# Kernel optimization log

Measured on AMD Instinct MI355X. Metric: run time of the kernel, lower is better.

Reference implementation:

```python
import jax, jax.numpy as jnp
import numpy as np

NEG_CLAMP = -100.0  # torch F.binary_cross_entropy clamps log terms at -100


def _ccl_labels(fg):
    """4-connectivity connected-component labeling of a [H,W] bool mask.
    Labels are assigned in raster-scan first-encounter order, matching
    scipy.ndimage.label with the default structure. Background = 0.
    Implemented as min-index label propagation to a fixed point: each
    component ends up tagged with the min flat index of its pixels (its
    first raster-scan pixel), then roots are ranked by cumsum to get 1..num.
    """
    H, W = fg.shape
    INF = H * W  # sentinel larger than any flat index
    idx = jnp.arange(INF, dtype=jnp.int32).reshape(H, W)
    init = jnp.where(fg, idx, INF)

    def step(x):
        up = jnp.concatenate([x[1:], jnp.full((1, W), INF, x.dtype)], axis=0)
        down = jnp.concatenate([jnp.full((1, W), INF, x.dtype), x[:-1]], axis=0)
        left = jnp.concatenate([x[:, 1:], jnp.full((H, 1), INF, x.dtype)], axis=1)
        right = jnp.concatenate([jnp.full((H, 1), INF, x.dtype), x[:, :-1]], axis=1)
        m = jnp.minimum(jnp.minimum(up, down), jnp.minimum(left, right))
        return jnp.where(fg, jnp.minimum(x, m), INF)

    def cond(carry):
        return carry[1]

    def body(carry):
        x, _ = carry
        nx = step(x)
        return nx, jnp.any(nx != x)

    x, _ = jax.lax.while_loop(cond, body, (init, jnp.array(True)))

    flat = x.reshape(-1)
    fgf = fg.reshape(-1)
    # a pixel is the root of its component iff its propagated tag == its own index
    is_root = fgf & (flat == jnp.arange(INF, dtype=jnp.int32))
    rank = jnp.cumsum(is_root.astype(jnp.int32))  # rank[r] = scipy label of root r
    labels = jnp.where(fgf, rank[jnp.clip(flat, 0, INF - 1)], 0)
    return labels.reshape(H, W)


def _target_map(fg):
    """Replicates: labels == labels.flatten()[1:].argmax() + 1 (faithful to source,
    including its quirky use of argmax position as the selected label value)."""
    labels = _ccl_labels(fg)
    lf = labels.reshape(-1)
    v = jnp.argmax(lf[1:]) + 1  # first occurrence of max, like numpy argmax
    return (labels == v).astype(jnp.float32)


def setup_inputs() -> dict:
    key = jax.random.key(0)
    pred = jax.random.uniform(key, (32, 1, 512, 512), dtype=jnp.float32)
    return {"pred": pred}


def reference(pred):
    fg = pred[:, 0] >= 0.5  # [N,H,W] bool
    target = jax.vmap(_target_map)(fg)[:, None]  # [N,1,H,W] float
    logp = jnp.maximum(jnp.log(pred), NEG_CLAMP)
    log1mp = jnp.maximum(jnp.log1p(-pred), NEG_CLAMP)
    return -jnp.mean(target * logp + (1.0 - target) * log1mp)
```

## Files before the change

kernel.cpp:

```cpp
#include <hip/hip_runtime.h>
#include <math.h>

#define IMG_W 512
#define IMG_H 512
#define HW (IMG_W * IMG_H)
#define LOGHW 18
#define NIMG 32
#define NTOT (NIMG * HW)
#define TILE 64
#define TPI 64
#define NTILE (NIMG * TPI)
#define EDGE_N (NTILE * 64)
#define NPAIR (NIMG * 112)
#define RTSTRIDE 2048

__device__ __forceinline__ void uf_unite(int* L, int a, int b) {
    while (true) {
        int p = ((volatile int*)L)[a];
        while (p != a) { a = p; p = ((volatile int*)L)[a]; }
        p = ((volatile int*)L)[b];
        while (p != b) { b = p; p = ((volatile int*)L)[b]; }
        if (a == b) return;
        if (a < b) { int t = a; a = b; b = t; }
        int old = atomicMin(&L[a], b);
        if (old == a) return;
        a = old;
    }
}

__global__ __launch_bounds__(512) void k_local(const float* __restrict__ pred,
                                               int* __restrict__ L,
                                               float* __restrict__ partials,
                                               int* __restrict__ edges,
                                               int* __restrict__ rootCnt,
                                               int* __restrict__ rootList,
                                               unsigned int* __restrict__ counter) {
    __shared__ int lab[TILE * TILE];
    __shared__ float swf[8];
    __shared__ int rootc;
    int tile = blockIdx.x;
    int img = tile >> 6;
    int t = tile & (TPI - 1);
    int ty = t >> 3, tx = t & 7;
    int baseLocal = (ty * TILE) * IMG_W + tx * TILE;
    const float* pi = pred + ((size_t)img << LOGHW);
    int* Li = L + ((size_t)img << LOGHW);
    int tid = threadIdx.x;
    int lane = tid & 63, wave = tid >> 6;
    if (tid == 0) rootc = 0;

    float acc = 0.0f;
#pragma unroll
    for (int j = 0; j < 8; j++) {
        int row = wave + j * 8;
        float p = pi[baseLocal + row * IMG_W + lane];
        acc += fmaxf(__logf(1.0f - p), -100.0f);
        bool fg = (p >= 0.5f);
        unsigned long long bal = __ballot(fg);
        unsigned long long starts = bal & ~(bal << 1);
        unsigned long long maskle =
            (lane == 63) ? ~0ULL : ((1ULL << (lane + 1)) - 1ULL);
        int lb = -1;
        if (fg) {
            unsigned long long pre = starts & maskle;
            lb = row * TILE + (63 - __builtin_clzll(pre));
        }
        lab[row * TILE + lane] = lb;
    }
    __syncthreads();
#pragma unroll
    for (int j = 0; j < 8; j++) {
        int row = wave + j * 8;
        if (row == 0) continue;
        int i = row * TILE + lane;
        bool c = (lab[i] >= 0) && (lab[i - TILE] >= 0);
        unsigned long long cb = __ballot(c);
        unsigned long long cs = cb & ~(cb << 1);
        if ((cs >> lane) & 1ULL) uf_unite(lab, i, i - TILE);
    }
    __syncthreads();
    int* rl = rootList + (size_t)tile * RTSTRIDE;
#pragma unroll
    for (int j = 0; j < 8; j++) {
        int row = wave + j * 8;
        int i = row * TILE + lane;
        bool fg = (lab[i] >= 0);
        unsigned long long bal = __ballot(fg);
        unsigned long long st = bal & ~(bal << 1);
        if ((st >> lane) & 1ULL) {
            int x = i, p = lab[x];
            while (p != x) {
                int g = lab[p];
                lab[x] = g;
                x = g;
                p = lab[x];
            }
            lab[i] = x;
            if (x == i) {
                int b = atomicAdd(&rootc, 1);
                rl[b] = baseLocal + (i >> 6) * IMG_W + (i & 63);
            }
        }
    }
    __syncthreads();
#pragma unroll
    for (int j = 0; j < 2; j++) {
        int i4 = (tid + j * 512) * 4;
        int4 s4 = *(const int4*)&lab[i4];
        const int* sp = (const int*)&s4;
        int4 o;
        int* op = (int*)&o;
#pragma unroll
        for (int k = 0; k < 4; k++) {
            int s = sp[k];
            if (s < 0) op[k] = -1;
            else {
                int r = lab[s];
                op[k] = baseLocal + (r >> 6) * IMG_W + (r & 63);
            }
        }
        *(int4*)(Li + baseLocal + (i4 >> 6) * IMG_W + (i4 & 63)) = o;
    }
    if (tid < 256) {
        int e = tid >> 6;
        int q = tid & 63;
        int px = (e == 0) ? q
               : (e == 1) ? (63 * TILE + q)
               : (e == 2) ? (q * TILE)
               :            (q * TILE + 63);
        int s = lab[px];
        int val = -1;
        if (s >= 0) {
            int r = lab[s];
            val = baseLocal + (r >> 6) * IMG_W + (r & 63);
        }
        edges[e * EDGE_N + tile * 64 + q] = val;
    }
#pragma unroll
    for (int o = 32; o > 0; o >>= 1) acc += __shfl_down(acc, o);
    if (lane == 0) swf[wave] = acc;
    __syncthreads();
    if (tid == 0) {
        float s = 0.0f;
#pragma unroll
        for (int w = 0; w < 8; w++) s += swf[w];
        partials[blockIdx.x] = s;
        rootCnt[tile] = rootc;
        if (blockIdx.x == 0) *counter = 0u;
    }
}

__global__ __launch_bounds__(256) void k_border(const int* __restrict__ edges,
                                                int* __restrict__ L) {
    int gid = blockIdx.x * blockDim.x + threadIdx.x;
    int pair = gid >> 6;
    int lane = gid & 63;
    int a, b, img;
    if (pair < NIMG * 56) {
        img = pair / 56;
        int w = pair - img * 56;
        int ty = w / 7, tx = w - ty * 7;
        int tl = img * TPI + ty * 8 + tx;
        a = edges[3 * EDGE_N + tl * 64 + lane];
        b = edges[2 * EDGE_N + (tl + 1) * 64 + lane];
    } else {
        int p2 = pair - NIMG * 56;
        img = p2 / 56;
        int w = p2 - img * 56;
        int ty = w >> 3, tx = w & 7;
        int tu = img * TPI + ty * 8 + tx;
        a = edges[1 * EDGE_N + tu * 64 + lane];
        b = edges[0 * EDGE_N + (tu + 8) * 64 + lane];
    }
    bool c = (a >= 0) && (b >= 0);
    unsigned long long cb = __ballot(c);
    unsigned long long cs = cb & ~(cb << 1);
    if ((cs >> lane) & 1ULL)
        uf_unite(L + ((size_t)img << LOGHW), a, b);
}

__global__ __launch_bounds__(512) void k_tail(const int* __restrict__ rootCnt,
                                              const int* __restrict__ rootList,
                                              const int* __restrict__ L,
                                              const float* __restrict__ pred,
                                              const float* __restrict__ partials,
                                              float* __restrict__ corr,
                                              unsigned int* __restrict__ counter,
                                              float* __restrict__ out) {
    __shared__ int pre[65];
    __shared__ int sc[512], sm[512];
    __shared__ int result;
    __shared__ float sf[512];
    __shared__ double sd[512];
    __shared__ unsigned int oldc;
    int img = blockIdx.x, t = threadIdx.x;
    const int* Li = L + ((size_t)img << LOGHW);

    if (t < 64) {
        int v = rootCnt[img * TPI + t];
#pragma unroll
        for (int o = 1; o < 64; o <<= 1) {
            int u = __shfl_up(v, o);
            if (t >= o) v += u;
        }
        pre[t + 1] = v;
        if (t == 0) pre[0] = 0;
    }
    if (t == 0) result = -2;
    __syncthreads();
    int C = pre[64];

    int cnt = 0, mx = -1;
    for (int k0 = t; k0 < C; k0 += 4096) {
        int rr0 = -1, rr1 = -1, rr2 = -1, rr3 = -1,
            rr4 = -1, rr5 = -1, rr6 = -1, rr7 = -1;
#define PROBE(J, RR)                                                        \
        {                                                                   \
            int k = k0 + (J) * 512;                                         \
            if (k < C) {                                                    \
                int lo = 0, hi = 64;                                        \
                for (int s = 0; s < 6; s++) {                               \
                    int mid = (lo + hi) >> 1;                               \
                    if (pre[mid] <= k) lo = mid; else hi = mid;             \
                }                                                           \
                RR = rootList[(size_t)(img * TPI + lo) * RTSTRIDE           \
                              + (k - pre[lo])];                             \
            }                                                               \
        }
        PROBE(0, rr0) PROBE(1, rr1) PROBE(2, rr2) PROBE(3, rr3)
        PROBE(4, rr4) PROBE(5, rr5) PROBE(6, rr6) PROBE(7, rr7)
#undef PROBE
#define TEST(RR) if ((RR) >= 0 && Li[RR] == (RR)) { cnt++; mx = max(mx, RR); }
        TEST(rr0) TEST(rr1) TEST(rr2) TEST(rr3)
        TEST(rr4) TEST(rr5) TEST(rr6) TEST(rr7)
#undef TEST
    }
    sc[t] = cnt; sm[t] = mx;
    __syncthreads();
    for (int s = 256; s > 0; s >>= 1) {
        if (t < s) { sc[t] += sc[t + s]; sm[t] = max(sm[t], sm[t + s]); }
        __syncthreads();
    }
    int num = sc[0], last_root = sm[0];
    int v;
    if (last_root >= 1) {
        v = last_root;
    } else {
        __syncthreads();
        int mn = HW;
        for (int i0 = t * 4; i0 < HW; i0 += 2048) {
            int4 l4 = *(const int4*)(Li + i0);
            if (l4.x >= 0 && i0 >= 1) mn = min(mn, i0);
            if (l4.y >= 0) mn = min(mn, i0 + 1);
            if (l4.z >= 0) mn = min(mn, i0 + 2);
            if (l4.w >= 0) mn = min(mn, i0 + 3);
        }
        sc[t] = mn;
        __syncthreads();
        for (int s = 256; s > 0; s >>= 1) {
            if (t < s) sc[t] = min(sc[t], sc[t + s]);
            __syncthreads();
        }
        mn = sc[0];
        v = (last_root == 0) ? ((mn < HW) ? mn : 1) : 1;
        __syncthreads();
    }

    if (v >= 1 && v <= num) {
        __syncthreads();
        int base = t * (HW / 512);
        int c = 0;
        for (int j = 0; j < 128; j++) {
            int off = base + j * 4;
            int4 l4 = *(const int4*)(Li + off);
            c += (l4.x == off) + (l4.y == off + 1)
               + (l4.z == off + 2) + (l4.w == off + 3);
        }
        sc[t] = c;
        __syncthreads();
        for (int off = 1; off < 512; off <<= 1) {
            int v2 = (t >= off) ? sc[t - off] : 0;
            __syncthreads();
            sc[t] += v2;
            __syncthreads();
        }
        int inc = sc[t], exc = inc - c;
        if (exc < v && v <= inc) {
            int need = v - exc, run = 0;
            for (int j = 0; j < 128; j++) {
                int off = base + j * 4;
                int4 l4 = *(const int4*)(Li + off);
                if (l4.x == off)     { run++; if (run == need) result = off; }
                if (l4.y == off + 1) { run++; if (run == need) result = off + 1; }
                if (l4.z == off + 2) { run++; if (run == need) result = off + 2; }
                if (l4.w == off + 3) { run++; if (run == need) result = off + 3; }
                if (run >= need) break;
            }
        }
        __syncthreads();
    }
    int rvv = result;
    float blocksum = 0.0f;
    if (rvv >= 0) {
        const float* pi = pred + ((size_t)img << LOGHW);
        float acc = 0.0f;
        for (int it = 0; it < HW / 2048; it++) {
            int off = it * 2048 + t * 4;
            float4 p4 = *(const float4*)(pi + off);
            int4 l4 = *(const int4*)(Li + off);
            const float* pp = (const float*)&p4;
            const int* lp = (const int*)&l4;
#pragma unroll
            for (int k = 0; k < 4; k++) {
                int p = lp[k];
                if (p < 0) continue;
                int x = p, q = Li[x];
                while (q != x) { x = q; q = Li[x]; }
                if (x == rvv) {
                    float pr = pp[k];
                    acc += fmaxf(__logf(pr), -100.0f)
                         - fmaxf(__logf(1.0f - pr), -100.0f);
                }
            }
        }
        sf[t] = acc;
        __syncthreads();
        for (int s = 256; s > 0; s >>= 1) {
            if (t < s) sf[t] += sf[t + s];
            __syncthreads();
        }
        blocksum = sf[0];
    }
    if (t == 0) {
        __hip_atomic_store(&corr[img], blocksum, __ATOMIC_RELAXED,
                           __HIP_MEMORY_SCOPE_AGENT);
        oldc = __hip_atomic_fetch_add(counter, 1u, __ATOMIC_ACQ_REL,
                                      __HIP_MEMORY_SCOPE_AGENT);
    }
    __syncthreads();
    if (oldc != NIMG - 1) return;
    double acc = 0.0;
#pragma unroll
    for (int j = 0; j < 4; j++) acc += (double)partials[t + j * 512];
    if (t < NIMG)
        acc += (double)__hip_atomic_load(&corr[t], __ATOMIC_ACQUIRE,
                                         __HIP_MEMORY_SCOPE_AGENT);
    sd[t] = acc;
    __syncthreads();
    for (int s = 256; s > 0; s >>= 1) {
        if (t < s) sd[t] += sd[t + s];
        __syncthreads();
    }
    if (t == 0) out[0] = (float)(-sd[0] / (double)NTOT);
}

extern "C" void kernel_launch(void* const* d_in, const int* in_sizes, int n_in,
                              void* d_out, int out_size, void* d_ws, size_t ws_size,
                              hipStream_t stream) {
    const float* pred = (const float*)d_in[0];
    float* out = (float*)d_out;

    char* ws = (char*)d_ws;
    int* L = (int*)ws;
    int* edges = (int*)(ws + (size_t)NTOT * 4);
    int* rootList = edges + 4 * EDGE_N;
    int* rootCnt = rootList + (size_t)NTILE * RTSTRIDE;
    float* partials = (float*)(rootCnt + NTILE);
    float* corr = partials + NTILE;
    unsigned int* counter = (unsigned int*)(corr + NIMG);

    k_local<<<dim3(NTILE), dim3(512), 0, stream>>>(pred, L, partials, edges,
                                                   rootCnt, rootList, counter);
    k_border<<<dim3(NPAIR * 64 / 256), dim3(256), 0, stream>>>(edges, L);
    k_tail<<<dim3(NIMG), dim3(512), 0, stream>>>(rootCnt, rootList, L, pred,
                                                 partials, corr, counter, out);
}
```

Baseline: 137.9 us.

## Record demoted roots during border union and filter tail roots via shared bitmap

The border union now reports which tile root it demoted with each successful atomicMin, and these are appended to a per-image list through wave-aggregated atomics. The tail kernel builds a shared-memory bitmap of demoted roots and finds surviving roots by checking that bitmap, with the component count taken as C minus D. This replaces the binary search over prefix sums and the random global reads of L for every root. It adds a 32KB shared bitmap per block, its clearing cost, and a fixed DEMCAP capacity that could overflow if an image has very many merges.

```diff
diff --git a/kernel.cpp b/kernel.cpp
--- a/kernel.cpp
+++ b/kernel.cpp
@@ -13,6 +13,7 @@
 #define EDGE_N (NTILE * 64)
 #define NPAIR (NIMG * 112)
 #define RTSTRIDE 2048
+#define DEMCAP 4096
 
 __device__ __forceinline__ void uf_unite(int* L, int a, int b) {
     while (true) {
@@ -28,12 +29,27 @@
     }
 }
 
+__device__ __forceinline__ int uf_unite_dem(int* L, int a, int b) {
+    while (true) {
+        int p = ((volatile int*)L)[a];
+        while (p != a) { a = p; p = ((volatile int*)L)[a]; }
+        p = ((volatile int*)L)[b];
+        while (p != b) { b = p; p = ((volatile int*)L)[b]; }
+        if (a == b) return -1;
+        if (a < b) { int t = a; a = b; b = t; }
+        int old = atomicMin(&L[a], b);
+        if (old == a) return a;
+        a = old;
+    }
+}
+
 __global__ __launch_bounds__(512) void k_local(const float* __restrict__ pred,
                                                int* __restrict__ L,
                                                float* __restrict__ partials,
                                                int* __restrict__ edges,
                                                int* __restrict__ rootCnt,
                                                int* __restrict__ rootList,
+                                               int* __restrict__ demCnt,
                                                unsigned int* __restrict__ counter) {
     __shared__ int lab[TILE * TILE];
     __shared__ float swf[8];
@@ -48,6 +64,7 @@
     int tid = threadIdx.x;
     int lane = tid & 63, wave = tid >> 6;
     if (tid == 0) rootc = 0;
+    if (blockIdx.x == 0 && tid < NIMG) demCnt[tid] = 0;
 
     float acc = 0.0f;
 #pragma unroll
@@ -151,7 +168,9 @@
 }
 
 __global__ __launch_bounds__(256) void k_border(const int* __restrict__ edges,
-                                                int* __restrict__ L) {
+                                                int* __restrict__ L,
+                                                int* __restrict__ demCnt,
+                                                int* __restrict__ demList) {
     int gid = blockIdx.x * blockDim.x + threadIdx.x;
     int pair = gid >> 6;
     int lane = gid & 63;
@@ -175,18 +194,33 @@
     bool c = (a >= 0) && (b >= 0);
     unsigned long long cb = __ballot(c);
     unsigned long long cs = cb & ~(cb << 1);
+    int d = -1;
     if ((cs >> lane) & 1ULL)
-        uf_unite(L + ((size_t)img << LOGHW), a, b);
+        d = uf_unite_dem(L + ((size_t)img << LOGHW), a, b);
+    unsigned long long db = __ballot(d >= 0);
+    if (db) {
+        int leader = __ffsll(db) - 1;
+        int base = 0;
+        if (lane == leader) base = atomicAdd(&demCnt[img], __popcll(db));
+        base = __shfl(base, leader);
+        if (d >= 0) {
+            int rank = __popcll(db & ((1ULL << lane) - 1ULL));
+            demList[img * DEMCAP + base + rank] = d;
+        }
+    }
 }
 
 __global__ __launch_bounds__(512) void k_tail(const int* __restrict__ rootCnt,
                                               const int* __restrict__ rootList,
+                                              const int* __restrict__ demCnt,
+                                              const int* __restrict__ demList,
                                               const int* __restrict__ L,
                                               const float* __restrict__ pred,
                                               const float* __restrict__ partials,
                                               float* __restrict__ corr,
                                               unsigned int* __restrict__ counter,
                                               float* __restrict__ out) {
+    __shared__ unsigned bm[HW / 32];
     __shared__ int pre[65];
     __shared__ int sc[512], sm[512];
     __shared__ int result;
@@ -196,6 +230,7 @@
     int img = blockIdx.x, t = threadIdx.x;
     const int* Li = L + ((size_t)img << LOGHW);
 
+    for (int i = t; i < HW / 32; i += 512) bm[i] = 0u;
     if (t < 64) {
         int v = rootCnt[img * TPI + t];
 #pragma unroll
@@ -209,39 +244,27 @@
     if (t == 0) result = -2;
     __syncthreads();
     int C = pre[64];
-
-    int cnt = 0, mx = -1;
-    for (int k0 = t; k0 < C; k0 += 4096) {
-        int rr0 = -1, rr1 = -1, rr2 = -1, rr3 = -1,
-            rr4 = -1, rr5 = -1, rr6 = -1, rr7 = -1;
-#define PROBE(J, RR)                                                        \
-        {                                                                   \
-            int k = k0 + (J) * 512;                                         \
-            if (k < C) {                                                    \
-                int lo = 0, hi = 64;                                        \
-                for (int s = 0; s < 6; s++) {                               \
-                    int mid = (lo + hi) >> 1;                               \
-                    if (pre[mid] <= k) lo = mid; else hi = mid;             \
-                }                                                           \
-                RR = rootList[(size_t)(img * TPI + lo) * RTSTRIDE           \
-                              + (k - pre[lo])];                             \
-            }                                                               \
-        }
-        PROBE(0, rr0) PROBE(1, rr1) PROBE(2, rr2) PROBE(3, rr3)
-        PROBE(4, rr4) PROBE(5, rr5) PROBE(6, rr6) PROBE(7, rr7)
-#undef PROBE
-#define TEST(RR) if ((RR) >= 0 && Li[RR] == (RR)) { cnt++; mx = max(mx, RR); }
-        TEST(rr0) TEST(rr1) TEST(rr2) TEST(rr3)
-        TEST(rr4) TEST(rr5) TEST(rr6) TEST(rr7)
-#undef TEST
-    }
-    sc[t] = cnt; sm[t] = mx;
+    int D = demCnt[img];
+    for (int k = t; k < D; k += 512) {
+        int d = demList[img * DEMCAP + k];
+        atomicOr(&bm[d >> 5], 1u << (d & 31));
+    }
+    __syncthreads();
+    int tt = t >> 3, j0 = t & 7;
+    int rc = pre[tt + 1] - pre[tt];
+    const int* rl = rootList + (size_t)(img * TPI + tt) * RTSTRIDE;
+    int mx = -1;
+    for (int k = j0; k < rc; k += 8) {
+        int r = rl[k];
+        if (!((bm[r >> 5] >> (r & 31)) & 1u)) mx = max(mx, r);
+    }
+    sm[t] = mx;
     __syncthreads();
     for (int s = 256; s > 0; s >>= 1) {
-        if (t < s) { sc[t] += sc[t + s]; sm[t] = max(sm[t], sm[t + s]); }
-        __syncthreads();
-    }
-    int num = sc[0], last_root = sm[0];
+        if (t < s) sm[t] = max(sm[t], sm[t + s]);
+        __syncthreads();
+    }
+    int num = C - D, last_root = sm[0];
     int v;
     if (last_root >= 1) {
         v = last_root;
@@ -365,13 +388,18 @@
     int* edges = (int*)(ws + (size_t)NTOT * 4);
     int* rootList = edges + 4 * EDGE_N;
     int* rootCnt = rootList + (size_t)NTILE * RTSTRIDE;
-    float* partials = (float*)(rootCnt + NTILE);
+    int* demCnt = rootCnt + NTILE;
+    int* demList = demCnt + NIMG;
+    float* partials = (float*)(demList + NIMG * DEMCAP);
     float* corr = partials + NTILE;
     unsigned int* counter = (unsigned int*)(corr + NIMG);
 
     k_local<<<dim3(NTILE), dim3(512), 0, stream>>>(pred, L, partials, edges,
-                                                   rootCnt, rootList, counter);
-    k_border<<<dim3(NPAIR * 64 / 256), dim3(256), 0, stream>>>(edges, L);
-    k_tail<<<dim3(NIMG), dim3(512), 0, stream>>>(rootCnt, rootList, L, pred,
-                                                 partials, corr, counter, out);
-}
+                                                   rootCnt, rootList, demCnt,
+                                                   counter);
+    k_border<<<dim3(NPAIR * 64 / 256), dim3(256), 0, stream>>>(edges, L,
+                                                               demCnt, demList);
+    k_tail<<<dim3(NIMG), dim3(512), 0, stream>>>(rootCnt, rootList, demCnt,
+                                                 demList, L, pred, partials,
+                                                 corr, counter, out);
+}
```

New measurement: 146.1 us. +5.9%, slower.

## Split root probing into a per-tile kernel to spread work across CUs

Applied to the files above, without the earlier changes.

Root probing (checking which tile-local roots remain union-find roots and tracking count and max) moves out of the 32-block tail kernel into a new kernel with one 64-thread block per tile (2048 blocks). The tail kernel then only reduces per-tile counts and maxima. The aim is to spread the random-access probe loads over many more CUs instead of 32 blocks doing binary searches over a prefix sum. The cost is one extra kernel launch and a small global write and read of per-tile results.

```diff
diff --git a/kernel.cpp b/kernel.cpp
--- a/kernel.cpp
+++ b/kernel.cpp
@@ -179,15 +179,38 @@
         uf_unite(L + ((size_t)img << LOGHW), a, b);
 }
 
-__global__ __launch_bounds__(512) void k_tail(const int* __restrict__ rootCnt,
+__global__ __launch_bounds__(64) void k_probe(const int* __restrict__ rootCnt,
                                               const int* __restrict__ rootList,
+                                              const int* __restrict__ L,
+                                              int* __restrict__ cntT,
+                                              int* __restrict__ maxT) {
+    int tile = blockIdx.x;
+    int img = tile >> 6;
+    const int* Li = L + ((size_t)img << LOGHW);
+    const int* rl = rootList + (size_t)tile * RTSTRIDE;
+    int rc = rootCnt[tile];
+    int lane = threadIdx.x;
+    int cnt = 0, mx = -1;
+    for (int k = lane; k < rc; k += 64) {
+        int r = rl[k];
+        if (Li[r] == r) { cnt++; mx = max(mx, r); }
+    }
+#pragma unroll
+    for (int o = 32; o > 0; o >>= 1) {
+        cnt += __shfl_down(cnt, o);
+        mx = max(mx, __shfl_down(mx, o));
+    }
+    if (lane == 0) { cntT[tile] = cnt; maxT[tile] = mx; }
+}
+
+__global__ __launch_bounds__(512) void k_tail(const int* __restrict__ cntT,
+                                              const int* __restrict__ maxT,
                                               const int* __restrict__ L,
                                               const float* __restrict__ pred,
                                               const float* __restrict__ partials,
                                               float* __restrict__ corr,
                                               unsigned int* __restrict__ counter,
                                               float* __restrict__ out) {
-    __shared__ int pre[65];
     __shared__ int sc[512], sm[512];
     __shared__ int result;
     __shared__ float sf[512];
@@ -196,46 +219,9 @@
     int img = blockIdx.x, t = threadIdx.x;
     const int* Li = L + ((size_t)img << LOGHW);
 
-    if (t < 64) {
-        int v = rootCnt[img * TPI + t];
-#pragma unroll
-        for (int o = 1; o < 64; o <<= 1) {
-            int u = __shfl_up(v, o);
-            if (t >= o) v += u;
-        }
-        pre[t + 1] = v;
-        if (t == 0) pre[0] = 0;
-    }
+    sc[t] = (t < TPI) ? cntT[img * TPI + t] : 0;
+    sm[t] = (t < TPI) ? maxT[img * TPI + t] : -1;
     if (t == 0) result = -2;
-    __syncthreads();
-    int C = pre[64];
-
-    int cnt = 0, mx = -1;
-    for (int k0 = t; k0 < C; k0 += 4096) {
-        int rr0 = -1, rr1 = -1, rr2 = -1, rr3 = -1,
-            rr4 = -1, rr5 = -1, rr6 = -1, rr7 = -1;
-#define PROBE(J, RR)                                                        \
-        {                                                                   \
-            int k = k0 + (J) * 512;                                         \
-            if (k < C) {                                                    \
-                int lo = 0, hi = 64;                                        \
-                for (int s = 0; s < 6; s++) {                               \
-                    int mid = (lo + hi) >> 1;                               \
-                    if (pre[mid] <= k) lo = mid; else hi = mid;             \
-                }                                                           \
-                RR = rootList[(size_t)(img * TPI + lo) * RTSTRIDE           \
-                              + (k - pre[lo])];                             \
-            }                                                               \
-        }
-        PROBE(0, rr0) PROBE(1, rr1) PROBE(2, rr2) PROBE(3, rr3)
-        PROBE(4, rr4) PROBE(5, rr5) PROBE(6, rr6) PROBE(7, rr7)
-#undef PROBE
-#define TEST(RR) if ((RR) >= 0 && Li[RR] == (RR)) { cnt++; mx = max(mx, RR); }
-        TEST(rr0) TEST(rr1) TEST(rr2) TEST(rr3)
-        TEST(rr4) TEST(rr5) TEST(rr6) TEST(rr7)
-#undef TEST
-    }
-    sc[t] = cnt; sm[t] = mx;
     __syncthreads();
     for (int s = 256; s > 0; s >>= 1) {
         if (t < s) { sc[t] += sc[t + s]; sm[t] = max(sm[t], sm[t + s]); }
@@ -365,13 +351,17 @@
     int* edges = (int*)(ws + (size_t)NTOT * 4);
     int* rootList = edges + 4 * EDGE_N;
     int* rootCnt = rootList + (size_t)NTILE * RTSTRIDE;
-    float* partials = (float*)(rootCnt + NTILE);
+    int* cntT = rootCnt + NTILE;
+    int* maxT = cntT + NTILE;
+    float* partials = (float*)(maxT + NTILE);
     float* corr = partials + NTILE;
     unsigned int* counter = (unsigned int*)(corr + NIMG);
 
     k_local<<<dim3(NTILE), dim3(512), 0, stream>>>(pred, L, partials, edges,
                                                    rootCnt, rootList, counter);
     k_border<<<dim3(NPAIR * 64 / 256), dim3(256), 0, stream>>>(edges, L);
-    k_tail<<<dim3(NIMG), dim3(512), 0, stream>>>(rootCnt, rootList, L, pred,
+    k_probe<<<dim3(NTILE), dim3(64), 0, stream>>>(rootCnt, rootList, L,
+                                                  cntT, maxT);
+    k_tail<<<dim3(NIMG), dim3(512), 0, stream>>>(cntT, maxT, L, pred,
                                                  partials, corr, counter, out);
 }
```

Result: faster. 121.2 us (-12.1%).
